# Kernel optimization log

Hardware: AMD Instinct MI355X
Metric: run time of the kernel (lower is better)

The kernel has to match this reference:

```python
import jax, jax.numpy as jnp
import numpy as np

NUM_INST = 32
EPS = 1e-5


def _conv(x, w, b, stride=1, pad=0):
    y = jax.lax.conv_general_dilated(
        x, w, (stride, stride), ((pad, pad), (pad, pad)),
        dimension_numbers=('NCHW', 'OIHW', 'NCHW'))
    return y + b[None, :, None, None]


def _deconv(x, w, b):
    # torch ConvTranspose2d(k=3, s=2, p=1, output_padding=1); w is (Cin, Cout, 3, 3)
    wf = jnp.flip(w, (2, 3)).transpose(1, 0, 2, 3)  # -> OIHW
    y = jax.lax.conv_general_dilated(
        x, wf, (1, 1), ((1, 2), (1, 2)), lhs_dilation=(2, 2),
        dimension_numbers=('NCHW', 'OIHW', 'NCHW'))
    return y + b[None, :, None, None]


def _inorm(x):
    m = x.mean((2, 3), keepdims=True)
    v = x.var((2, 3), keepdims=True)  # biased, matches InstanceNorm2d
    return (x - m) * jax.lax.rsqrt(v + EPS)


def _rpad(x, p=3):
    return jnp.pad(x, ((0, 0), (0, 0), (p, p), (p, p)), mode='reflect')


def _backbone(input, w0, b0, w1, b1, w2, b2, w3, b3, w4, b4,
              w5, b5, w6, b6, w7, b7, w8, b8, w9, b9):
    x = jax.nn.relu(_inorm(_conv(_rpad(input), w0, b0)))          # [B,16,H,W]
    x = jax.nn.relu(_inorm(_conv(x, w1, b1, stride=2, pad=1)))    # [B,32,H/2,..]
    x = jax.nn.relu(_inorm(_conv(x, w2, b2, stride=2, pad=1)))    # [B,64,H/4,..]
    x = jax.nn.relu(_inorm(_conv(x, w3, b3, stride=2, pad=1)))    # [B,128,H/8,..]
    x = jax.nn.relu(_inorm(_conv(x, w4, b4, stride=2, pad=1)))    # [B,256,H/16,..]
    x = jax.nn.relu(_inorm(_deconv(x, w5, b5)))                   # [B,128,H/8,..]
    x = jax.nn.relu(_inorm(_deconv(x, w6, b6)))                   # [B,64,H/4,..]
    x = jax.nn.relu(_inorm(_deconv(x, w7, b7)))                   # [B,32,H/2,..]
    x = jax.nn.relu(_inorm(_deconv(x, w8, b8)))                   # [B,16,H,W]
    return jnp.tanh(_conv(_rpad(x), w9, b9))                      # [B,Cout,H,W]


def _segment_mean(outputs, inst):
    # outputs [B,C,H,W]; inst [B,1,H,W] int labels shared across the batch.
    B, C, H, W = outputs.shape
    seg = inst.reshape(-1)                                # [B*H*W]
    feats = outputs.transpose(0, 2, 3, 1).reshape(-1, C)  # [B*H*W, C]
    sums = jax.ops.segment_sum(feats, seg, num_segments=NUM_INST)
    counts = jax.ops.segment_sum(jnp.ones((feats.shape[0],), feats.dtype), seg,
                                 num_segments=NUM_INST)
    means = sums / jnp.maximum(counts, 1.0)[:, None]      # [NUM_INST, C]
    out = means[seg].reshape(B, H, W, C).transpose(0, 3, 1, 2)
    return out


def setup_inputs() -> dict:
    key = jax.random.key(0)
    ks = jax.random.split(key, 16)
    B, Cin, Cout, H, W = 4, 3, 3, 512, 512
    inp = {
        'input': jax.random.normal(ks[0], (B, Cin, H, W), jnp.float32),
        'inst': jax.random.randint(ks[1], (B, 1, H, W), 0, NUM_INST, jnp.int32),
    }
    std = 0.02
    # conv weights OIHW; deconv weights torch-style (Cin, Cout, kH, kW)
    shapes = [
        ('w0', (16, Cin, 7, 7)), ('w1', (32, 16, 3, 3)), ('w2', (64, 32, 3, 3)),
        ('w3', (128, 64, 3, 3)), ('w4', (256, 128, 3, 3)),
        ('w5', (256, 128, 3, 3)), ('w6', (128, 64, 3, 3)),
        ('w7', (64, 32, 3, 3)), ('w8', (32, 16, 3, 3)), ('w9', (Cout, 16, 7, 7)),
    ]
    bias_dims = [16, 32, 64, 128, 256, 128, 64, 32, 16, Cout]
    for i, (name, shp) in enumerate(shapes):
        inp[name] = std * jax.random.normal(ks[2 + i], shp, jnp.float32)
        inp['b%d' % i] = jnp.zeros((bias_dims[i],), jnp.float32)
    return inp


def reference(input, inst, w0, b0, w1, b1, w2, b2, w3, b3, w4, b4,
              w5, b5, w6, b6, w7, b7, w8, b8, w9, b9):
    outputs = _backbone(input, w0, b0, w1, b1, w2, b2, w3, b3, w4, b4,
                        w5, b5, w6, b6, w7, b7, w8, b8, w9, b9)
    return _segment_mean(outputs, inst)
```

## Files before the change

kernel.cpp:

```cpp
#include <hip/hip_runtime.h>
#include <math.h>

#define EPS_F 1e-5f

typedef __attribute__((ext_vector_type(8))) short short8;
typedef __attribute__((ext_vector_type(4))) float f32x4;
typedef __attribute__((ext_vector_type(8))) unsigned short ushort8;

__device__ __forceinline__ int reflect512(int v) {
    v = v < 0 ? -v : v;
    return v >= 512 ? 1022 - v : v;
}

__device__ __forceinline__ ushort f2bf(float f) {
    union { float f; unsigned u; } v; v.f = f;
    unsigned r = v.u + 0x7FFFu + ((v.u >> 16) & 1u);
    return (ushort)(r >> 16);
}
__device__ __forceinline__ float bf2f(ushort u) {
    union { unsigned u; float f; } v; v.u = (unsigned)u << 16;
    return v.f;
}

__device__ __forceinline__ float fast_tanh(float x) {
    float cx = fminf(fmaxf(x, -9.f), 9.f);
    float e  = __builtin_amdgcn_exp2f(cx * 2.8853900817779268f);
    return (e - 1.f) * __builtin_amdgcn_rcpf(e + 1.f);
}

template<int CIN, int COUT, bool DEC>
__device__ __forceinline__ void wp_mid(
    const float* __restrict__ w, ushort* __restrict__ dst, int i)
{
    constexpr int CIP = ((CIN + 31) / 32) * 32;
    int ci = i % CIP;
    int oc = (i / CIP) % COUT;
    int t  = i / (CIP * COUT);
    float x = 0.f;
    if (ci < CIN)
        x = DEC ? w[((size_t)ci * COUT + oc) * 9 + t]
                : w[((size_t)oc * CIN + ci) * 9 + t];
    dst[i] = f2bf(x);
}

template<bool L9>
__device__ __forceinline__ void wp_7(
    const float* __restrict__ w, ushort* __restrict__ dst, int i)
{
    constexpr int CINR  = L9 ? 16 : 3;
    constexpr int COUTR = L9 ? 3  : 16;
    int j   = i & 7;
    int oc  = (i >> 3) & 15;
    int kqe = (i >> 7) & 3;
    int cn  = i >> 9;
    int k = cn * 32 + kqe * 8 + j;
    int t, ci;
    if (L9) { t = k >> 4; ci = k & 15; } else { t = k >> 3; ci = k & 7; }
    float x = (t < 49 && oc < COUTR && ci < CINR)
              ? w[((size_t)oc * CINR + ci) * 49 + t] : 0.f;
    dst[i] = f2bf(x);
}

struct WprepArgs {
    const float* w[10];
    ushort* d[10];
};

__global__ __launch_bounds__(256) void wprep_all(WprepArgs a)
{
    int bi = blockIdx.x;
    int t  = threadIdx.x;
    if      (bi < 36)   wp_mid<16,  32,  false>(a.w[1], a.d[1], (bi        ) * 256 + t);
    else if (bi < 108)  wp_mid<32,  64,  false>(a.w[2], a.d[2], (bi - 36   ) * 256 + t);
    else if (bi < 396)  wp_mid<64,  128, false>(a.w[3], a.d[3], (bi - 108  ) * 256 + t);
    else if (bi < 1548) wp_mid<128, 256, false>(a.w[4], a.d[4], (bi - 396  ) * 256 + t);
    else if (bi < 2700) wp_mid<256, 128, true >(a.w[5], a.d[5], (bi - 1548 ) * 256 + t);
    else if (bi < 2988) wp_mid<128, 64,  true >(a.w[6], a.d[6], (bi - 2700 ) * 256 + t);
    else if (bi < 3060) wp_mid<64,  32,  true >(a.w[7], a.d[7], (bi - 2988 ) * 256 + t);
    else if (bi < 3078) wp_mid<32,  16,  true >(a.w[8], a.d[8], (bi - 3060 ) * 256 + t);
    else if (bi < 3104) wp_7<false>(a.w[0], a.d[0], (bi - 3078) * 256 + t);
    else                wp_7<true >(a.w[9], a.d[9], (bi - 3104) * 256 + t);
}

template<int CIN, int COUT, int WIN, int MODE, int NWN, int MSUB, int RT, int CT>
__global__ __launch_bounds__(256) void mfconv(
    const ushort* __restrict__ in, const ushort* __restrict__ wbf,
    const float* __restrict__ bias, ushort* __restrict__ out,
    const float* __restrict__ stats_in, float invHWin,
    float* __restrict__ stats_out)
{
    constexpr int HWIN = WIN * WIN;
    constexpr int WOUT = (MODE == 0) ? (WIN / 2) : (WIN * 2);
    constexpr int HWOUT = WOUT * WOUT;
    constexpr int NMG = 4 / NWN;
    constexpr int NOC = NWN * 16;
    constexpr int M = NMG * MSUB * 16;
    static_assert(M == RT * CT, "tile mismatch");
    constexpr int SPAN = (MODE == 0) ? WOUT : WIN;
    constexpr int XC = SPAN / CT, YC = SPAN / RT;
    constexpr int NG = COUT / NOC;
    constexpr int NR = (MODE == 0) ? (2 * RT + 1) : (RT + 1);
    constexpr int NCO = (MODE == 0) ? (2 * CT + 1) : (CT + 1);
    constexpr int NPIX = NR * NCO;
    constexpr int CIP = ((CIN + 31) / 32) * 32;
    constexpr int NQ = (MODE == 0) ? 1 : 4;
    constexpr int LPW = 36;
    constexpr int NPOUT = (MODE == 0 ? 1 : 4) * M;
    constexpr int NOCP = NOC + 8;

    constexpr int TDY[9] = {1,1,1,0,0,0,0,0,0};
    constexpr int TDX[9] = {1,0,0,1,0,0,1,0,0};
    constexpr int TQ [9] = {3,2,3,1,0,1,3,2,3};

    extern __shared__ ushort sa[];
    __shared__ float mrall[CIP][2];
    __shared__ float sred[4][16][2];

    const int tid = threadIdx.x;
    const int lane = tid & 63, wv = tid >> 6;
    const int ln = lane & 15, kq = lane >> 4;
    const int wn = wv % NWN, wm = wv / NWN;
    const int grp = tid & 3;

    int bi = blockIdx.x;
    const int xc = bi % XC; bi /= XC;
    const int yc = bi % YC; bi /= YC;
    const int g  = bi % NG;
    const int b  = bi / NG;

    const int ocg = g * NOC + wn * 16 + ln;
    const float b0 = bias[ocg];
    f32x4 acc[NQ][MSUB];
    #pragma unroll
    for (int q = 0; q < NQ; q++)
        #pragma unroll
        for (int s = 0; s < MSUB; s++)
            acc[q][s] = (f32x4){b0, b0, b0, b0};

    for (int e = tid; e < CIP; e += 256) {
        float m = 0.f, r = 0.f;
        if (e < CIN) {
            int c = b * CIN + e;
            float s1 = stats_in[2 * c], s2 = stats_in[2 * c + 1];
            m = s1 * invHWin;
            r = rsqrtf(fmaf(s2, invHWin, -m * m) + EPS_F);
        }
        mrall[e][0] = m; mrall[e][1] = r;
    }

    const ushort* inb = in + (size_t)b * HWIN * CIN;

    for (int c0 = 0; c0 < CIP; c0 += 32) {
        __syncthreads();
        const int ch0 = c0 + 8 * grp;
        float m8[8], r8[8];
        #pragma unroll
        for (int j = 0; j < 8; j++) { m8[j] = mrall[ch0 + j][0]; r8[j] = mrall[ch0 + j][1]; }
        for (int pix = tid >> 2; pix < NPIX; pix += 64) {
            int pr = pix / NCO, pc = pix - pr * NCO;
            int gy, gx;
            if (MODE == 0) { gy = 2 * (yc * RT) - 1 + pr; gx = 2 * (xc * CT) - 1 + pc; }
            else           { gy = yc * RT + pr;           gx = xc * CT + pc; }
            ushort8 pk;
            #pragma unroll
            for (int j = 0; j < 8; j++) pk[j] = 0;
            if ((unsigned)gy < (unsigned)WIN && (unsigned)gx < (unsigned)WIN && ch0 < CIN) {
                ushort8 raw = *(const ushort8*)(inb + (size_t)(gy * WIN + gx) * CIN + ch0);
                #pragma unroll
                for (int j = 0; j < 8; j++) {
                    float x = bf2f(raw[j]);
                    pk[j] = f2bf(fmaxf((x - m8[j]) * r8[j], 0.f));
                }
            }
            *(ushort8*)&sa[pix * LPW + grp * 8] = pk;
        }
        __syncthreads();
        #pragma unroll
        for (int t = 0; t < 9; t++) {
            short8 bfr = *(const short8*)&wbf[((size_t)t * COUT + ocg) * CIP + c0 + kq * 8];
            #pragma unroll
            for (int s = 0; s < MSUB; s++) {
                const int mb = wm * MSUB * 16 + s * 16;
                const int r = mb / CT, cb = mb % CT;
                int pix;
                if (MODE == 0) pix = (t / 3 + 2 * r) * NCO + 2 * (cb + ln) + t % 3;
                else           pix = (TDY[t] + r) * NCO + cb + ln + TDX[t];
                short8 afr = *(const short8*)&sa[pix * LPW + kq * 8];
                int qd = (MODE == 0) ? 0 : TQ[t];
                acc[qd][s] = __builtin_amdgcn_mfma_f32_16x16x32_bf16(afr, bfr, acc[qd][s], 0, 0, 0);
            }
        }
    }

    float s1 = 0.f, s2 = 0.f;
    #pragma unroll
    for (int q = 0; q < NQ; q++)
        #pragma unroll
        for (int s = 0; s < MSUB; s++)
            #pragma unroll
            for (int rg = 0; rg < 4; rg++) {
                float v = acc[q][s][rg];
                s1 += v; s2 = fmaf(v, v, s2);
            }
    s1 += __shfl_xor(s1, 16); s2 += __shfl_xor(s2, 16);
    s1 += __shfl_xor(s1, 32); s2 += __shfl_xor(s2, 32);
    if (lane < 16) { sred[wv][lane][0] = s1; sred[wv][lane][1] = s2; }

    __syncthreads();
    const int ocl = wn * 16 + ln;
    if (MODE == 0) {
        #pragma unroll
        for (int s = 0; s < MSUB; s++)
            #pragma unroll
            for (int rg = 0; rg < 4; rg++) {
                const int m = wm * MSUB * 16 + s * 16 + kq * 4 + rg;
                sa[m * NOCP + ocl] = f2bf(acc[0][s][rg]);
            }
    } else {
        #pragma unroll
        for (int q = 0; q < 4; q++) {
            const int dy = q >> 1, dx = q & 1;
            #pragma unroll
            for (int s = 0; s < MSUB; s++)
                #pragma unroll
                for (int rg = 0; rg < 4; rg++) {
                    const int m = wm * MSUB * 16 + s * 16 + kq * 4 + rg;
                    const int r = m / CT, c = m % CT;
                    const int lp = (2 * r + dy) * (2 * CT) + 2 * c + dx;
                    sa[lp * NOCP + ocl] = f2bf(acc[q][s][rg]);
                }
        }
    }
    __syncthreads();

    ushort* ob = out + (size_t)b * HWOUT * COUT + g * NOC;
    for (int e = tid; e < (NPOUT * NOC) / 8; e += 256) {
        int u = e * 8;
        int lp = u / NOC, co = u % NOC;
        int gp;
        if (MODE == 0) {
            int r = lp / CT, c = lp % CT;
            gp = (yc * RT + r) * WOUT + xc * CT + c;
        } else {
            int r2 = lp / (2 * CT), x2 = lp % (2 * CT);
            gp = (2 * (yc * RT) + r2) * WOUT + 2 * (xc * CT) + x2;
        }
        *(ushort8*)&ob[(size_t)gp * COUT + co] = *(const ushort8*)&sa[lp * NOCP + co];
    }

    if (tid < NOC) {
        int wnn = tid >> 4, oc = tid & 15;
        float t1 = 0.f, t2 = 0.f;
        #pragma unroll
        for (int k = 0; k < NMG; k++) {
            t1 += sred[wnn + k * NWN][oc][0];
            t2 += sred[wnn + k * NWN][oc][1];
        }
        int cix = b * COUT + g * NOC + wnn * 16 + oc;
        atomicAdd(&stats_out[2 * cix],     t1);
        atomicAdd(&stats_out[2 * cix + 1], t2);
    }
}

template<bool BFIN, bool SEG>
__global__ __launch_bounds__(256, 4) void conv7x(
    const float* __restrict__ inf, const ushort* __restrict__ inb16,
    const ushort* __restrict__ wpk, const float* __restrict__ bias,
    ushort* __restrict__ out,
    const float* __restrict__ stats_in, float invHWin,
    float* __restrict__ stats_out,
    const int* __restrict__ inst, float* __restrict__ segacc)
{
    constexpr int W = 512, HW = 512 * 512;
    constexpr int NCHUNK = BFIN ? 25 : 13;
    constexpr int STR = BFIN ? 20 : 12;
    constexpr int SASZ = BFIN ? (980 * 20) : 12288;

    __shared__ ushort sa[SASZ];
    __shared__ float mr[16][2];
    __shared__ float segl[SEG ? 128 : 1];
    __shared__ float sred[4][16][2];

    const int tid = threadIdx.x;
    const int lane = tid & 63, wv = tid >> 6;
    const int ln = lane & 15, kq = lane >> 4;

    int bi = blockIdx.x;
    const int xc = bi & 7;
    const int yr = (bi >> 3) & 63;
    const int b  = bi >> 9;
    const int y0 = yr * 8, x0 = xc * 64;

    if constexpr (SEG) { if (tid < 128) segl[tid] = 0.f; }
    if constexpr (BFIN) {
        if (tid < 16) {
            int c = b * 16 + tid;
            float s1 = stats_in[2 * c], s2 = stats_in[2 * c + 1];
            float m = s1 * invHWin;
            mr[tid][0] = m;
            mr[tid][1] = rsqrtf(fmaf(s2, invHWin, -m * m) + EPS_F);
        }
        __syncthreads();
        const int h = tid & 1;
        float m8[8], r8[8];
        #pragma unroll
        for (int j = 0; j < 8; j++) { m8[j] = mr[8 * h + j][0]; r8[j] = mr[8 * h + j][1]; }
        const ushort* inb = inb16 + (size_t)b * HW * 16;
        for (int pix = tid >> 1; pix < 980; pix += 128) {
            int pr = pix / 70, pc = pix - pr * 70;
            int gy = reflect512(y0 - 3 + pr);
            int gx = reflect512(x0 - 3 + pc);
            ushort8 raw = *(const ushort8*)(inb + (size_t)(gy * W + gx) * 16 + 8 * h);
            ushort8 pk;
            #pragma unroll
            for (int j = 0; j < 8; j++) {
                float x = bf2f(raw[j]);
                pk[j] = f2bf(fmaxf((x - m8[j]) * r8[j], 0.f));
            }
            *(ushort8*)&sa[pix * STR + 8 * h] = pk;
        }
    } else {
        const float* p0 = inf + (size_t)b * 3 * HW;
        for (int pix = tid; pix < 980; pix += 256) {
            int pr = pix / 70, pc = pix - pr * 70;
            int gy = reflect512(y0 - 3 + pr);
            int gx = reflect512(x0 - 3 + pc);
            const float* p = p0 + gy * W + gx;
            ushort8 pk;
            #pragma unroll
            for (int j = 0; j < 8; j++) pk[j] = 0;
            pk[0] = f2bf(p[0]); pk[1] = f2bf(p[HW]); pk[2] = f2bf(p[2 * (size_t)HW]);
            *(ushort8*)&sa[pix * STR] = pk;
        }
    }
    __syncthreads();

    const float b0 = (ln < (BFIN ? 3 : 16)) ? bias[ln] : 0.f;
    f32x4 acc[8];
    #pragma unroll
    for (int s = 0; s < 8; s++) acc[s] = (f32x4){b0, b0, b0, b0};

    const ushort* wpp = wpk + ((size_t)kq * 16 + ln) * 8;
    short8 wcur = *(const short8*)wpp;

    #pragma unroll
    for (int cn = 0; cn < NCHUNK; cn++) {
        short8 wnxt;
        if (cn + 1 < NCHUNK)
            wnxt = *(const short8*)(wpp + (size_t)(cn + 1) * 512);
        int t, off;
        if constexpr (BFIN) { t = 2 * cn + (kq >> 1); off = (kq & 1) * 8; }
        else                { t = 4 * cn + kq;        off = 0; }
        t = t > 48 ? 48 : t;
        const int ty = t / 7, tx = t - ty * 7;
        short8 afr[8];
        #pragma unroll
        for (int s = 0; s < 8; s++) {
            int m = wv * 128 + s * 16 + ln;
            int r = m >> 6, c = m & 63;
            afr[s] = *(const short8*)&sa[((r + ty) * 70 + c + tx) * STR + off];
        }
        #pragma unroll
        for (int s = 0; s < 8; s++)
            acc[s] = __builtin_amdgcn_mfma_f32_16x16x32_bf16(afr[s], wcur, acc[s], 0, 0, 0);
        if (cn + 1 < NCHUNK) wcur = wnxt;
    }

    if constexpr (SEG) {
        float* sf = (float*)sa;
        __syncthreads();
        if (ln < 3) {
            #pragma unroll
            for (int s = 0; s < 8; s++)
                #pragma unroll
                for (int rg = 0; rg < 4; rg++) {
                    int m = wv * 128 + s * 16 + kq * 4 + rg;
                    sf[m * 5 + ln] = acc[s][rg];
                }
        }
        __syncthreads();
        const int* ib = inst + ((size_t)b << 18);
        for (int p2 = tid; p2 < 512; p2 += 256) {
            int r = p2 >> 6, c = p2 & 63;
            int lab = ib[(y0 + r) * W + x0 + c] & 31;
            atomicAdd(&segl[lab * 4 + 0], fast_tanh(sf[p2 * 5 + 0]));
            atomicAdd(&segl[lab * 4 + 1], fast_tanh(sf[p2 * 5 + 1]));
            atomicAdd(&segl[lab * 4 + 2], fast_tanh(sf[p2 * 5 + 2]));
            atomicAdd(&segl[lab * 4 + 3], 1.f);
        }
        __syncthreads();
        if (tid < 128) {
            float v = segl[tid];
            if (v != 0.f) atomicAdd(&segacc[tid], v);
        }
    } else {
        float s1 = 0.f, s2 = 0.f;
        #pragma unroll
        for (int s = 0; s < 8; s++)
            #pragma unroll
            for (int rg = 0; rg < 4; rg++) {
                float v = acc[s][rg];
                s1 += v; s2 = fmaf(v, v, s2);
            }
        s1 += __shfl_xor(s1, 16); s2 += __shfl_xor(s2, 16);
        s1 += __shfl_xor(s1, 32); s2 += __shfl_xor(s2, 32);
        if (lane < 16) { sred[wv][lane][0] = s1; sred[wv][lane][1] = s2; }

        __syncthreads();
        #pragma unroll
        for (int s = 0; s < 8; s++)
            #pragma unroll
            for (int rg = 0; rg < 4; rg++) {
                int m = wv * 128 + s * 16 + kq * 4 + rg;
                sa[m * 24 + ln] = f2bf(acc[s][rg]);
            }
        __syncthreads();
        ushort* ob = out + (size_t)b * HW * 16;
        for (int e = tid; e < 1024; e += 256) {
            int u = e * 8;
            int lp = u >> 4, co = u & 15;
            int gp = (y0 + (lp >> 6)) * W + x0 + (lp & 63);
            *(ushort8*)&ob[(size_t)gp * 16 + co] = *(const ushort8*)&sa[lp * 24 + co];
        }
        if (tid < 16) {
            float t1 = 0.f, t2 = 0.f;
            #pragma unroll
            for (int k = 0; k < 4; k++) { t1 += sred[k][tid][0]; t2 += sred[k][tid][1]; }
            int cix = b * 16 + tid;
            atomicAdd(&stats_out[2 * cix],     t1);
            atomicAdd(&stats_out[2 * cix + 1], t2);
        }
    }
}

#define HW9 262144
__global__ void seg_final(const float* __restrict__ acc, float* __restrict__ means)
{
    int i = threadIdx.x;
    if (i < 96) {
        int s = i / 3, c = i - s * 3;
        means[i] = acc[s * 4 + c] / fmaxf(acc[s * 4 + 3], 1.f);
    }
}

__global__ __launch_bounds__(256) void seg_scatter(
    const int* __restrict__ inst, const float* __restrict__ means,
    float* __restrict__ out)
{
    int p   = blockIdx.x * 256 + threadIdx.x;
    int b   = p >> 18;
    int r   = p & (HW9 - 1);
    int lab = inst[p] & 31;
    float* ob = out + (size_t)b * 3 * HW9;
    ob[r]           = means[lab * 3 + 0];
    ob[HW9 + r]     = means[lab * 3 + 1];
    ob[2 * HW9 + r] = means[lab * 3 + 2];
}

extern "C" void kernel_launch(void* const* d_in, const int* in_sizes, int n_in,
                              void* d_out, int out_size, void* d_ws, size_t ws_size,
                              hipStream_t stream)
{
    const float* x_in = (const float*)d_in[0];
    const int*   inst = (const int*)d_in[1];
    const float* W_[10];
    const float* Bs[10];
    for (int i = 0; i < 10; i++) {
        W_[i] = (const float*)d_in[2 + 2 * i];
        Bs[i] = (const float*)d_in[3 + 2 * i];
    }
    float* out = (float*)d_out;

    ushort* Ab  = (ushort*)d_ws;
    ushort* Bb2 = Ab + (size_t)16777216;
    float*  st  = (float*)(Bb2 + (size_t)8388608);
    const int coff[9] = {0, 128, 384, 896, 1920, 3968, 4992, 5504, 5760};
    float* s_[9];
    for (int i = 0; i < 9; i++) s_[i] = st + coff[i];
    float* segacc = st + 5888;
    float* means  = st + 6016;
    ushort* wb = (ushort*)(st + 8192);
    const size_t OW1 = 0, OW2 = 9216, OW3 = 27648, OW4 = 101376,
                 OW5 = 396288, OW6 = 691200, OW7 = 764928, OW8 = 783360;
    ushort* wb0 = wb + 790000;
    ushort* wb9 = wb0 + 6656;

    hipMemsetAsync(st, 0, 6016 * sizeof(float), stream);

    WprepArgs wa;
    for (int i = 0; i < 10; i++) wa.w[i] = W_[i];
    wa.d[0] = wb0;
    wa.d[1] = wb + OW1; wa.d[2] = wb + OW2; wa.d[3] = wb + OW3; wa.d[4] = wb + OW4;
    wa.d[5] = wb + OW5; wa.d[6] = wb + OW6; wa.d[7] = wb + OW7; wa.d[8] = wb + OW8;
    wa.d[9] = wb9;
    wprep_all<<<dim3(3154), dim3(256), 0, stream>>>(wa);

    conv7x<false, false><<<dim3(2048), dim3(256), 0, stream>>>(
        x_in, nullptr, wb0, Bs[0], Ab, nullptr, 0.f, s_[0], nullptr, nullptr);

    mfconv<16, 32, 512, 0, 2, 4, 4, 32><<<dim3(2048), dim3(256), 42120, stream>>>(
        Ab, wb + OW1, Bs[1], Bb2, s_[0], 1.f / 262144.f, s_[1]);

    mfconv<32, 64, 256, 0, 2, 4, 4, 32><<<dim3(1024), dim3(256), 42120, stream>>>(
        Bb2, wb + OW2, Bs[2], Ab, s_[1], 1.f / 65536.f, s_[2]);

    mfconv<64, 128, 128, 0, 2, 4, 4, 32><<<dim3(512), dim3(256), 42120, stream>>>(
        Ab, wb + OW3, Bs[3], Bb2, s_[2], 1.f / 16384.f, s_[3]);

    mfconv<128, 256, 64, 0, 2, 2, 2, 32><<<dim3(512), dim3(256), 23400, stream>>>(
        Bb2, wb + OW4, Bs[4], Ab, s_[3], 1.f / 4096.f, s_[4]);

    mfconv<256, 128, 32, 1, 1, 1, 2, 32><<<dim3(512), dim3(256), 12288, stream>>>(
        Ab, wb + OW5, Bs[5], Bb2, s_[4], 1.f / 1024.f, s_[5]);

    mfconv<128, 64, 64, 1, 2, 2, 2, 32><<<dim3(512), dim3(256), 20480, stream>>>(
        Bb2, wb + OW6, Bs[6], Ab, s_[5], 1.f / 4096.f, s_[6]);

    mfconv<64, 32, 128, 1, 2, 2, 2, 32><<<dim3(1024), dim3(256), 20480, stream>>>(
        Ab, wb + OW7, Bs[7], Bb2, s_[6], 1.f / 16384.f, s_[7]);

    mfconv<32, 16, 256, 1, 1, 2, 2, 64><<<dim3(2048), dim3(256), 24576, stream>>>(
        Bb2, wb + OW8, Bs[8], Ab, s_[7], 1.f / 65536.f, s_[8]);

    conv7x<true, true><<<dim3(2048), dim3(256), 0, stream>>>(
        nullptr, Ab, wb9, Bs[9], nullptr, s_[8], 1.f / 262144.f, nullptr, inst, segacc);

    seg_final<<<dim3(1), dim3(96), 0, stream>>>(segacc, means);
    seg_scatter<<<dim3(4096), dim3(256), 0, stream>>>(inst, means, out);
}
```

Baseline: 515.3 us.

## Reuse A fragments across kernel rows in final 7x7 conv via row-pair weight packing

```diff
diff --git a/kernel.cpp b/kernel.cpp
--- a/kernel.cpp
+++ b/kernel.cpp
@@ -47,17 +47,24 @@
 __device__ __forceinline__ void wp_7(
     const float* __restrict__ w, ushort* __restrict__ dst, int i)
 {
-    constexpr int CINR  = L9 ? 16 : 3;
-    constexpr int COUTR = L9 ? 3  : 16;
     int j   = i & 7;
     int oc  = (i >> 3) & 15;
     int kqe = (i >> 7) & 3;
     int cn  = i >> 9;
-    int k = cn * 32 + kqe * 8 + j;
-    int t, ci;
-    if (L9) { t = k >> 4; ci = k & 15; } else { t = k >> 3; ci = k & 7; }
-    float x = (t < 49 && oc < COUTR && ci < CINR)
-              ? w[((size_t)oc * CINR + ci) * 49 + t] : 0.f;
+    float x = 0.f;
+    if (L9) {
+        int k = kqe * 8 + j;
+        int rowsel = k >> 4, ci = k & 15;
+        int p = cn / 7, tx = cn - 7 * p;
+        int trow = 2 * p + rowsel;
+        if (trow < 7 && oc < 3)
+            x = w[((size_t)oc * 16 + ci) * 49 + trow * 7 + tx];
+    } else {
+        int k = cn * 32 + kqe * 8 + j;
+        int t = k >> 3, ci = k & 7;
+        if (t < 49 && ci < 3)
+            x = w[((size_t)oc * 3 + ci) * 49 + t];
+    }
     dst[i] = f2bf(x);
 }
 
@@ -272,7 +279,6 @@
     const int* __restrict__ inst, float* __restrict__ segacc)
 {
     constexpr int W = 512, HW = 512 * 512;
-    constexpr int NCHUNK = BFIN ? 25 : 13;
     constexpr int STR = BFIN ? 20 : 12;
     constexpr int SASZ = BFIN ? (980 * 20) : 12288;
 
@@ -340,30 +346,44 @@
     #pragma unroll
     for (int s = 0; s < 8; s++) acc[s] = (f32x4){b0, b0, b0, b0};
 
-    const ushort* wpp = wpk + ((size_t)kq * 16 + ln) * 8;
-    short8 wcur = *(const short8*)wpp;
-
-    #pragma unroll
-    for (int cn = 0; cn < NCHUNK; cn++) {
-        short8 wnxt;
-        if (cn + 1 < NCHUNK)
-            wnxt = *(const short8*)(wpp + (size_t)(cn + 1) * 512);
-        int t, off;
-        if constexpr (BFIN) { t = 2 * cn + (kq >> 1); off = (kq & 1) * 8; }
-        else                { t = 4 * cn + kq;        off = 0; }
-        t = t > 48 ? 48 : t;
-        const int ty = t / 7, tx = t - ty * 7;
-        short8 afr[8];
-        #pragma unroll
-        for (int s = 0; s < 8; s++) {
-            int m = wv * 128 + s * 16 + ln;
-            int r = m >> 6, c = m & 63;
-            afr[s] = *(const short8*)&sa[((r + ty) * 70 + c + tx) * STR + off];
-        }
-        #pragma unroll
-        for (int s = 0; s < 8; s++)
-            acc[s] = __builtin_amdgcn_mfma_f32_16x16x32_bf16(afr[s], wcur, acc[s], 0, 0, 0);
-        if (cn + 1 < NCHUNK) wcur = wnxt;
+    if constexpr (BFIN) {
+        const int c0 = wv * 16;
+        const int abase   = (((kq >> 1) * 70) + c0 + ln) * STR + (kq & 1) * 8;
+        const int abase13 = (13 * 70 + c0 + ln) * STR + (kq & 1) * 8;
+        const ushort* wp9 = wpk + ((size_t)kq * 16 + ln) * 8;
+        #pragma unroll
+        for (int tx = 0; tx < 7; tx++) {
+            short8 bfr[4];
+            #pragma unroll
+            for (int p = 0; p < 4; p++)
+                bfr[p] = *(const short8*)(wp9 + (size_t)(p * 7 + tx) * 512);
+            #pragma unroll
+            for (int R = 0; R < 14; R++) {
+                short8 afr = (R < 13)
+                    ? *(const short8*)&sa[abase + (R * 70 + tx) * STR]
+                    : *(const short8*)&sa[abase13 + tx * STR];
+                #pragma unroll
+                for (int p = 0; p < 4; p++) {
+                    const int s = R - 2 * p;
+                    if (s >= 0 && s < 8)
+                        acc[s] = __builtin_amdgcn_mfma_f32_16x16x32_bf16(afr, bfr[p], acc[s], 0, 0, 0);
+                }
+            }
+        }
+    } else {
+        for (int cn = 0; cn < 13; cn++) {
+            short8 bfr = *(const short8*)&wpk[((size_t)(cn * 4 + kq) * 16 + ln) * 8];
+            int t = 4 * cn + kq;
+            t = t > 48 ? 48 : t;
+            const int ty = t / 7, tx = t - ty * 7;
+            #pragma unroll
+            for (int s = 0; s < 8; s++) {
+                int m = wv * 128 + s * 16 + ln;
+                int r = m >> 6, c = m & 63;
+                short8 afr = *(const short8*)&sa[((r + ty) * 70 + c + tx) * STR];
+                acc[s] = __builtin_amdgcn_mfma_f32_16x16x32_bf16(afr, bfr, acc[s], 0, 0, 0);
+            }
+        }
     }
 
     if constexpr (SEG) {
@@ -374,7 +394,7 @@
             for (int s = 0; s < 8; s++)
                 #pragma unroll
                 for (int rg = 0; rg < 4; rg++) {
-                    int m = wv * 128 + s * 16 + kq * 4 + rg;
+                    int m = s * 64 + wv * 16 + kq * 4 + rg;
                     sf[m * 5 + ln] = acc[s][rg];
                 }
         }
@@ -493,7 +513,7 @@
     wa.d[1] = wb + OW1; wa.d[2] = wb + OW2; wa.d[3] = wb + OW3; wa.d[4] = wb + OW4;
     wa.d[5] = wb + OW5; wa.d[6] = wb + OW6; wa.d[7] = wb + OW7; wa.d[8] = wb + OW8;
     wa.d[9] = wb9;
-    wprep_all<<<dim3(3154), dim3(256), 0, stream>>>(wa);
+    wprep_all<<<dim3(3160), dim3(256), 0, stream>>>(wa);
 
     conv7x<false, false><<<dim3(2048), dim3(256), 0, stream>>>(
         x_in, nullptr, wb0, Bs[0], Ab, nullptr, 0.f, s_[0], nullptr, nullptr);
```

Result: faster. 504.7 us (-2.1%).
